# Kernel tuning notes

Hardware: AMD Instinct MI355X
Metric: run time of the kernel (lower is better)

The kernel has to match this reference:

```python
import jax, jax.numpy as jnp
import numpy as np

B, N, C, DIN, DOUT = 16, 65536, 256, 16, 16  # ratio = N // C = 256 nodes per cluster


def setup_inputs() -> dict:
    key = jax.random.key(0)
    k1, k2, k3, k4, k5 = jax.random.split(key, 5)
    stdv = 1.0 / np.sqrt(DOUT)
    x = jax.random.normal(k1, (B, N, DIN), dtype=jnp.float32)
    # parameters, pre-reshaped: torch w_diag (in*out, C) with out-major io axis -> (out, in, C)
    w_diag = jax.random.uniform(k2, (DOUT, DIN, C), jnp.float32, -stdv, stdv)
    w_off = jax.random.uniform(k3, (DOUT, DIN, C, C), jnp.float32, -stdv, stdv)
    b1 = jax.random.uniform(k4, (DOUT,), jnp.float32, -stdv, stdv)
    # flatten_ids(cluster_ids): a permutation putting each cluster's nodes contiguous
    permute_ids = jax.random.permutation(k5, N)
    return {"x": x, "w_diag": w_diag, "w_off": w_off, "b1": b1, "permute_ids": permute_ids}


def reference(x, w_diag, w_off, b1, permute_ids):
    # Faithful to: W = rearrange(kron(diag_embed(w_diag), I_r)) + (1/N) rearrange(kron(w_off, 1_{rxr}))
    # out = inv_permute( reshape( W @ flatten(permute(x)) ) ) + b1,
    # computed via the block-constant structure instead of materializing the (Dout*N, Din*N) W.
    Bq, Nn, Din = x.shape
    Dout, _, Cc = w_diag.shape
    ratio = Nn // Cc
    inv_permute = jnp.argsort(permute_ids)
    xp = x[:, permute_ids, :]                       # (B, N, Din), cluster-contiguous
    xc = xp.reshape(Bq, Cc, ratio, Din)             # (B, C, r, Din)
    # diagonal blocks: per-cluster Din->Dout mixing, identity over within-cluster index
    out_diag = jnp.einsum('oic,bcri->bcro', w_diag, xc)   # (B, C, r, Dout)
    # off blocks: constant within each (cluster j, cluster k) block -> use cluster sums
    s = xc.sum(axis=2)                              # (B, C, Din)
    out_off = jnp.einsum('oick,bki->bco', w_off, s) / Nn  # (B, C, Dout)
    out = out_diag + out_off[:, :, None, :]         # broadcast over within-cluster index
    out = out.reshape(Bq, Nn, Dout)[:, inv_permute, :] + b1[None, None, :]
    return out
```

## Files before the change

kernel.cpp:

```cpp
#include <hip/hip_runtime.h>

#define B_    16
#define N_    65536
#define C_    256
#define DIN_  16
#define DOUT_ 16


__global__ __launch_bounds__(256) void k_sum_prep(
    const float* __restrict__ x, const float* __restrict__ w_diag,
    const int* __restrict__ P, float* __restrict__ s,
    float* __restrict__ wd_t, int* __restrict__ c_of_n)
{
    int bid = blockIdx.x;
    int t = threadIdx.x;
    if (bid >= B_ * C_) {
        int r = bid - B_ * C_;
        if (r < 256) {
            int o = r >> 4, i = r & 15;
            wd_t[t * 256 + i * 16 + o] = w_diag[r * C_ + t];
        } else {
            int k = r - 256;
            c_of_n[P[k * 256 + t]] = k;
        }
        return;
    }
    int b = bid >> 8;
    int k = bid & (C_ - 1);
    int q  = t & 3;
    int rg = t >> 2;
    float4 acc = make_float4(0.f, 0.f, 0.f, 0.f);
    const int jbase = k << 8;
    #pragma unroll
    for (int m = 0; m < 4; ++m) {
        int n = P[jbase + rg + 64 * m];
        const float4* row =
            reinterpret_cast<const float4*>(x + ((size_t)(b * N_ + n)) * DIN_);
        float4 v = row[q];
        acc.x += v.x; acc.y += v.y; acc.z += v.z; acc.w += v.w;
    }
    #pragma unroll
    for (int mask = 4; mask <= 32; mask <<= 1) {
        acc.x += __shfl_xor(acc.x, mask, 64);
        acc.y += __shfl_xor(acc.y, mask, 64);
        acc.z += __shfl_xor(acc.z, mask, 64);
        acc.w += __shfl_xor(acc.w, mask, 64);
    }
    __shared__ float4 part[4][4];
    int lane = t & 63, wave = t >> 6;
    if (lane < 4) part[wave][lane] = acc;
    __syncthreads();
    if (t < 16) {
        int qq = t >> 2, comp = t & 3;
        float v = 0.f;
        #pragma unroll
        for (int w = 0; w < 4; ++w) {
            const float* p = reinterpret_cast<const float*>(&part[w][qq]);
            v += p[comp];
        }
        int i = qq * 4 + comp;
        s[i * (B_ * C_) + b * C_ + k] = v;
    }
}

__global__ __launch_bounds__(256) void k_off(
    const float* __restrict__ w_off, const float* __restrict__ s,
    const float* __restrict__ b1, float* __restrict__ off)
{
    int c  = blockIdx.x >> 2;
    int og = blockIdx.x & 3;
    int t  = threadIdx.x;
    float acc[64];
    #pragma unroll
    for (int z = 0; z < 64; ++z) acc[z] = 0.f;

    for (int i = 0; i < DIN_; ++i) {
        float wv[4];
        #pragma unroll
        for (int o4 = 0; o4 < 4; ++o4) {
            int o = og * 4 + o4;
            wv[o4] = w_off[((size_t)((o * DIN_ + i) * C_ + c)) * C_ + t];
        }
        #pragma unroll
        for (int b = 0; b < B_; ++b) {
            float sv = s[i * (B_ * C_) + b * C_ + t];
            #pragma unroll
            for (int o4 = 0; o4 < 4; ++o4) acc[b * 4 + o4] += wv[o4] * sv;
        }
    }

    __shared__ float red[8][256];
    const float invN = 1.0f / (float)N_;
    #pragma unroll
    for (int rd = 0; rd < 8; ++rd) {
        __syncthreads();
        #pragma unroll
        for (int oo = 0; oo < 8; ++oo) red[oo][t] = acc[rd * 8 + oo];
        __syncthreads();
        int grp = t >> 5;
        int seg = t & 31;
        float p = 0.f;
        #pragma unroll
        for (int j = 0; j < 8; ++j) p += red[grp][seg * 8 + j];
        #pragma unroll
        for (int d = 16; d > 0; d >>= 1) p += __shfl_down(p, d, 32);
        if (seg == 0) {
            int outid = rd * 8 + grp;
            int b  = outid >> 2, o4 = outid & 3;
            int o  = og * 4 + o4;
            off[((b << 8) + c) * DOUT_ + o] = p * invN + b1[o];
        }
    }
}

__global__ __launch_bounds__(256) void k_apply_seq(
    const float* __restrict__ x, const int* __restrict__ c_of_n,
    const float* __restrict__ wd_t, const float* __restrict__ off,
    float* __restrict__ out)
{
    int t = threadIdx.x;
    int lr = t >> 2, q = t & 3;
    int n = blockIdx.x * 64 + lr;
    int c = c_of_n[n];

    const float4* wd4 = reinterpret_cast<const float4*>(wd_t);
    float4 wds[16];
    #pragma unroll
    for (int i = 0; i < 16; ++i) wds[i] = wd4[c * 64 + i * 4 + q];

    const float4* x4   = reinterpret_cast<const float4*>(x);
    const float4* off4 = reinterpret_cast<const float4*>(off);
    float4* out4       = reinterpret_cast<float4*>(out);

    #pragma unroll 2
    for (int b = 0; b < B_; ++b) {
        size_t rowbase = ((size_t)(b * N_ + n)) * 4;
        float4 x0 = x4[rowbase + 0];
        float4 x1 = x4[rowbase + 1];
        float4 x2 = x4[rowbase + 2];
        float4 x3 = x4[rowbase + 3];
        float4 acc = off4[((size_t)((b << 8) + c)) * 4 + q];
        float xv[16];
        xv[0]=x0.x; xv[1]=x0.y; xv[2]=x0.z; xv[3]=x0.w;
        xv[4]=x1.x; xv[5]=x1.y; xv[6]=x1.z; xv[7]=x1.w;
        xv[8]=x2.x; xv[9]=x2.y; xv[10]=x2.z; xv[11]=x2.w;
        xv[12]=x3.x; xv[13]=x3.y; xv[14]=x3.z; xv[15]=x3.w;
        #pragma unroll
        for (int i = 0; i < 16; ++i) {
            acc.x += xv[i] * wds[i].x;
            acc.y += xv[i] * wds[i].y;
            acc.z += xv[i] * wds[i].z;
            acc.w += xv[i] * wds[i].w;
        }
        out4[rowbase + q] = acc;
    }
}

extern "C" void kernel_launch(void* const* d_in, const int* in_sizes, int n_in,
                              void* d_out, int out_size, void* d_ws, size_t ws_size,
                              hipStream_t stream) {
    const float* x      = (const float*)d_in[0];
    const float* w_diag = (const float*)d_in[1];
    const float* w_off  = (const float*)d_in[2];
    const float* b1     = (const float*)d_in[3];
    const int*   P      = (const int*)d_in[4];
    float* out    = (float*)d_out;
    float* s      = (float*)d_ws;
    float* off    = s + 65536;
    float* wd_t   = off + 65536;
    int*   c_of_n = (int*)(wd_t + 65536);

    k_sum_prep<<<B_ * C_ + 512, 256, 0, stream>>>(x, w_diag, P, s, wd_t, c_of_n);
    k_off<<<C_ * 4, 256, 0, stream>>>(w_off, s, b1, off);
    k_apply_seq<<<N_ / 64, 256, 0, stream>>>(x, c_of_n, wd_t, off, out);
}
```

Baseline: 213.5 us.

## Restructure k_off with LDS double-buffered cluster sums and float4 weight loads

Rewrites the off-block kernel so each block handles 8 output channels instead of 4, halving the grid. The cluster sums are staged in double-buffered shared memory with a register prefetch of the next input channel, and w_off is read as float4 so each thread covers 4 source clusters. The shared-memory tree reduction is replaced by a full-wave shuffle reduction. This aims to cut redundant global reads of s and the reduction overhead, at the cost of a 32 KB LDS footprint per block, a barrier every input channel, and fewer blocks in flight.

```diff
diff --git a/kernel.cpp b/kernel.cpp
--- a/kernel.cpp
+++ b/kernel.cpp
@@ -67,49 +67,64 @@
     const float* __restrict__ w_off, const float* __restrict__ s,
     const float* __restrict__ b1, float* __restrict__ off)
 {
-    int c  = blockIdx.x >> 2;
-    int og = blockIdx.x & 3;
+    int c  = (int)blockIdx.x >> 1;
+    int og = (int)blockIdx.x & 1;
     int t  = threadIdx.x;
-    float acc[64];
+    int kq = t & 63;
+    int op = t >> 6;
+    int o0 = og * 8 + op * 2;
+
+    __shared__ float4 slds[2][1024];
+
+    const float4* s4 = reinterpret_cast<const float4*>(s);
     #pragma unroll
-    for (int z = 0; z < 64; ++z) acc[z] = 0.f;
+    for (int j = 0; j < 4; ++j) slds[0][t + 256 * j] = s4[t + 256 * j];
+    __syncthreads();
 
+    const float* w0p = w_off + ((size_t)(o0 * DIN_) * C_ + c) * C_ + kq * 4;
+    const float* w1p = w0p + (size_t)DIN_ * C_ * C_;
+
+    float acc[32];
+    #pragma unroll
+    for (int z = 0; z < 32; ++z) acc[z] = 0.f;
+
+    #pragma unroll 2
     for (int i = 0; i < DIN_; ++i) {
-        float wv[4];
-        #pragma unroll
-        for (int o4 = 0; o4 < 4; ++o4) {
-            int o = og * 4 + o4;
-            wv[o4] = w_off[((size_t)((o * DIN_ + i) * C_ + c)) * C_ + t];
+        int cur = i & 1;
+        float4 pf0, pf1, pf2, pf3;
+        if (i < DIN_ - 1) {
+            const float4* src = s4 + (i + 1) * 1024;
+            pf0 = src[t];       pf1 = src[t + 256];
+            pf2 = src[t + 512]; pf3 = src[t + 768];
         }
+        float4 w0 = *reinterpret_cast<const float4*>(w0p + (size_t)i * (C_ * C_));
+        float4 w1 = *reinterpret_cast<const float4*>(w1p + (size_t)i * (C_ * C_));
         #pragma unroll
         for (int b = 0; b < B_; ++b) {
-            float sv = s[i * (B_ * C_) + b * C_ + t];
-            #pragma unroll
-            for (int o4 = 0; o4 < 4; ++o4) acc[b * 4 + o4] += wv[o4] * sv;
+            float4 sv = slds[cur][b * 64 + kq];
+            acc[b * 2 + 0] += w0.x * sv.x + w0.y * sv.y + w0.z * sv.z + w0.w * sv.w;
+            acc[b * 2 + 1] += w1.x * sv.x + w1.y * sv.y + w1.z * sv.z + w1.w * sv.w;
         }
+        if (i < DIN_ - 1) {
+            float4* dst = slds[cur ^ 1];
+            dst[t] = pf0;       dst[t + 256] = pf1;
+            dst[t + 512] = pf2; dst[t + 768] = pf3;
+        }
+        __syncthreads();
     }
 
-    __shared__ float red[8][256];
-    const float invN = 1.0f / (float)N_;
     #pragma unroll
-    for (int rd = 0; rd < 8; ++rd) {
-        __syncthreads();
+    for (int z = 0; z < 32; ++z) {
+        float v = acc[z];
         #pragma unroll
-        for (int oo = 0; oo < 8; ++oo) red[oo][t] = acc[rd * 8 + oo];
-        __syncthreads();
-        int grp = t >> 5;
-        int seg = t & 31;
-        float p = 0.f;
-        #pragma unroll
-        for (int j = 0; j < 8; ++j) p += red[grp][seg * 8 + j];
-        #pragma unroll
-        for (int d = 16; d > 0; d >>= 1) p += __shfl_down(p, d, 32);
-        if (seg == 0) {
-            int outid = rd * 8 + grp;
-            int b  = outid >> 2, o4 = outid & 3;
-            int o  = og * 4 + o4;
-            off[((b << 8) + c) * DOUT_ + o] = p * invN + b1[o];
-        }
+        for (int mask = 1; mask <= 32; mask <<= 1)
+            v += __shfl_xor(v, mask, 64);
+        acc[z] = v;
+    }
+    if (kq < 32) {
+        int b = kq >> 1;
+        int o = o0 + (kq & 1);
+        off[((b << 8) + c) * DOUT_ + o] = acc[kq] * (1.0f / (float)N_) + b1[o];
     }
 }
 
@@ -171,6 +186,6 @@
     int*   c_of_n = (int*)(wd_t + 65536);
 
     k_sum_prep<<<B_ * C_ + 512, 256, 0, stream>>>(x, w_diag, P, s, wd_t, c_of_n);
-    k_off<<<C_ * 4, 256, 0, stream>>>(w_off, s, b1, off);
+    k_off<<<C_ * 2, 256, 0, stream>>>(w_off, s, b1, off);
     k_apply_seq<<<N_ / 64, 256, 0, stream>>>(x, c_of_n, wd_t, off, out);
 }
```

After: 207.3 us. 2.9% less time.

## Restructure off-block GEMV with float4 loads, LDS double-buffered sums, and shuffle-fold reduction

Applied to the files above, without the earlier changes.

The k_off kernel now launches one block per cluster instead of four, with each wave owning four output channels. It reads w_off and the cluster sums as float4, double-buffers the sums through LDS and prefetches registers two steps ahead. The shared-memory tree reduction is replaced by a butterfly shuffle fold that leaves one output per lane. This targets the bandwidth-bound 64MB w_off read and cuts barrier and LDS traffic, in exchange for more register pressure and fewer blocks in flight.

```diff
diff --git a/kernel.cpp b/kernel.cpp
--- a/kernel.cpp
+++ b/kernel.cpp
@@ -67,50 +67,92 @@
     const float* __restrict__ w_off, const float* __restrict__ s,
     const float* __restrict__ b1, float* __restrict__ off)
 {
-    int c  = blockIdx.x >> 2;
-    int og = blockIdx.x & 3;
-    int t  = threadIdx.x;
+    const int c  = blockIdx.x;
+    const int t  = threadIdx.x;
+    const int kq = t & 63;
+    const int wq = t >> 6;
+
+    __shared__ float4 slds[2][1024];
+
+    const float4* s4 = reinterpret_cast<const float4*>(s);
+    const float4* w4 = reinterpret_cast<const float4*>(w_off);
+
+    int wbase[4];
+    #pragma unroll
+    for (int o4 = 0; o4 < 4; ++o4)
+        wbase[o4] = (wq * 4 + o4) * 262144 + c * 64 + kq;
+
     float acc[64];
     #pragma unroll
     for (int z = 0; z < 64; ++z) acc[z] = 0.f;
 
-    for (int i = 0; i < DIN_; ++i) {
-        float wv[4];
-        #pragma unroll
-        for (int o4 = 0; o4 < 4; ++o4) {
-            int o = og * 4 + o4;
-            wv[o4] = w_off[((size_t)((o * DIN_ + i) * C_ + c)) * C_ + t];
-        }
-        #pragma unroll
-        for (int b = 0; b < B_; ++b) {
-            float sv = s[i * (B_ * C_) + b * C_ + t];
-            #pragma unroll
-            for (int o4 = 0; o4 < 4; ++o4) acc[b * 4 + o4] += wv[o4] * sv;
-        }
-    }
-
-    __shared__ float red[8][256];
-    const float invN = 1.0f / (float)N_;
-    #pragma unroll
-    for (int rd = 0; rd < 8; ++rd) {
-        __syncthreads();
-        #pragma unroll
-        for (int oo = 0; oo < 8; ++oo) red[oo][t] = acc[rd * 8 + oo];
-        __syncthreads();
-        int grp = t >> 5;
-        int seg = t & 31;
-        float p = 0.f;
-        #pragma unroll
-        for (int j = 0; j < 8; ++j) p += red[grp][seg * 8 + j];
-        #pragma unroll
-        for (int d = 16; d > 0; d >>= 1) p += __shfl_down(p, d, 32);
-        if (seg == 0) {
-            int outid = rd * 8 + grp;
-            int b  = outid >> 2, o4 = outid & 3;
-            int o  = og * 4 + o4;
-            off[((b << 8) + c) * DOUT_ + o] = p * invN + b1[o];
-        }
-    }
+    float4 sA[4], sB[4], wA[4], wB[4], s0[4];
+
+    #pragma unroll
+    for (int j = 0; j < 4; ++j) s0[j] = s4[t + 256 * j];
+    #pragma unroll
+    for (int o4 = 0; o4 < 4; ++o4) wA[o4] = w4[wbase[o4]];
+    #pragma unroll
+    for (int j = 0; j < 4; ++j) sA[j] = s4[1024 + t + 256 * j];
+    #pragma unroll
+    for (int j = 0; j < 4; ++j) slds[0][t + 256 * j] = s0[j];
+    __syncthreads();
+
+#define K2_BODY(I, WC, WN, SR, SI, RB, WBUF)                                   \
+    {                                                                          \
+        if ((I) + 2 < DIN_) {                                                  \
+            _Pragma("unroll")                                                  \
+            for (int j = 0; j < 4; ++j)                                        \
+                SI[j] = s4[((I) + 2) * 1024 + t + 256 * j];                    \
+        }                                                                      \
+        if ((I) + 1 < DIN_) {                                                  \
+            _Pragma("unroll")                                                  \
+            for (int o4 = 0; o4 < 4; ++o4)                                     \
+                WN[o4] = w4[wbase[o4] + ((I) + 1) * 16384];                    \
+        }                                                                      \
+        _Pragma("unroll")                                                      \
+        for (int b = 0; b < 16; ++b) {                                         \
+            float4 sv = slds[RB][b * 64 + kq];                                 \
+            _Pragma("unroll")                                                  \
+            for (int o4 = 0; o4 < 4; ++o4)                                     \
+                acc[o4 * 16 + b] += WC[o4].x * sv.x + WC[o4].y * sv.y          \
+                                  + WC[o4].z * sv.z + WC[o4].w * sv.w;         \
+        }                                                                      \
+        if ((I) + 1 < DIN_) {                                                  \
+            _Pragma("unroll")                                                  \
+            for (int j = 0; j < 4; ++j)                                        \
+                slds[WBUF][t + 256 * j] = SR[j];                               \
+            __syncthreads();                                                   \
+        }                                                                      \
+    }
+
+    #pragma unroll 1
+    for (int ih = 0; ih < DIN_ / 2; ++ih) {
+        const int i0 = ih * 2;
+        K2_BODY(i0,     wA, wB, sA, sB, 0, 1)
+        K2_BODY(i0 + 1, wB, wA, sB, sA, 1, 0)
+    }
+#undef K2_BODY
+
+#define FOLD(MASK, CNT)                                                        \
+    {                                                                          \
+        const bool hi_ = (kq & (MASK)) != 0;                                   \
+        _Pragma("unroll")                                                      \
+        for (int j = 0; j < (CNT); ++j) {                                      \
+            float keep = hi_ ? acc[j + (CNT)] : acc[j];                        \
+            float send = hi_ ? acc[j] : acc[j + (CNT)];                        \
+            acc[j] = keep + __shfl_xor(send, (MASK), 64);                      \
+        }                                                                      \
+    }
+    FOLD(1, 32) FOLD(2, 16) FOLD(4, 8) FOLD(8, 4) FOLD(16, 2) FOLD(32, 1)
+#undef FOLD
+
+    int j = ((kq >> 5) & 1) | ((kq >> 3) & 2) | ((kq >> 1) & 4)
+          | ((kq << 1) & 8) | ((kq << 3) & 16) | ((kq << 5) & 32);
+    int b  = j & 15;
+    int o4 = j >> 4;
+    int o  = wq * 4 + o4;
+    off[((b << 8) + c) * DOUT_ + o] = acc[0] * (1.0f / (float)N_) + b1[o];
 }
 
 __global__ __launch_bounds__(256) void k_apply_seq(
@@ -171,6 +213,6 @@
     int*   c_of_n = (int*)(wd_t + 65536);
 
     k_sum_prep<<<B_ * C_ + 512, 256, 0, stream>>>(x, w_diag, P, s, wd_t, c_of_n);
-    k_off<<<C_ * 4, 256, 0, stream>>>(w_off, s, b1, off);
+    k_off<<<C_, 256, 0, stream>>>(w_off, s, b1, off);
     k_apply_seq<<<N_ / 64, 256, 0, stream>>>(x, c_of_n, wd_t, off, out);
 }
```

Result: slower. 224.6 us (+5.2%).
